# Kernel tuning notes

Measured on AMD Instinct MI355X. Metric: run time of the kernel, lower is better.

Reference implementation:

```python
import jax, jax.numpy as jnp
import numpy as np

B, T, IN_DIM, HID_DIM = 64, 1024, 256, 256


def setup_inputs() -> dict:
    key = jax.random.key(0)
    ks = jax.random.split(key, 5)
    glorot = np.sqrt(6.0 / (IN_DIM + HID_DIM * 2)).astype(np.float32)
    def W(k):
        return jax.random.uniform(k, (IN_DIM + HID_DIM, HID_DIM), jnp.float32, -glorot, glorot)
    return {
        "x": jax.random.normal(ks[0], (B, T, IN_DIM), jnp.float32),
        "W_i": W(ks[1]), "b_i": jnp.zeros((HID_DIM,), jnp.float32),
        "W_f": W(ks[2]), "b_f": jnp.zeros((HID_DIM,), jnp.float32),
        "W_o": W(ks[3]), "b_o": jnp.zeros((HID_DIM,), jnp.float32),
        "W_c": W(ks[4]), "b_c": jnp.zeros((HID_DIM,), jnp.float32),
    }


def reference(x, W_i, b_i, W_f, b_f, W_o, b_o, W_c, b_c):
    # x: [B, T, in_dim] -> time-major [T, B, in_dim]
    xt = jnp.transpose(x, (1, 0, 2))
    batch = x.shape[0]
    c0 = jnp.zeros((batch, HID_DIM), x.dtype)
    h0 = jnp.zeros((batch, HID_DIM), x.dtype)

    def step(carry, x_t):
        c, h = carry
        hx = jnp.concatenate([h, x_t], axis=1)  # [B, hid+in]
        i = jax.nn.sigmoid(hx @ W_i + b_i)
        f = jax.nn.sigmoid(hx @ W_f + b_f)
        o = jax.nn.sigmoid(hx @ W_o + b_o)
        c_new = f * c + i * jnp.tanh(hx @ W_c + b_c)
        h_new = o * jnp.tanh(c_new)
        return (c_new, h_new), h_new

    _, outputs = jax.lax.scan(step, (c0, h0), xt)
    return outputs  # [T, B, hid_dim]
```

## Files before the change

kernel.cpp:

```cpp
#include <hip/hip_runtime.h>
#include <hip/hip_fp16.h>
#include <cstdint>

typedef _Float16 f16x8 __attribute__((ext_vector_type(8)));
typedef _Float16 half2_t __attribute__((ext_vector_type(2)));
typedef float f32x4 __attribute__((ext_vector_type(4)));
typedef uint32_t u32x4 __attribute__((ext_vector_type(4)));


#define XG_OFF    0ULL
#define XG_BYTES  134217728ULL
#define AP_OFF    (XG_OFF + XG_BYTES)
#define AP_BYTES  33554432ULL
#define BP_OFF    (AP_OFF + AP_BYTES)
#define BP_BYTES  524288ULL
#define WHP_OFF   (BP_OFF + BP_BYTES)
#define WHP_BYTES 524288ULL
#define BIAS_OFF  (WHP_OFF + WHP_BYTES)

#define KRQ 28
#define KLB 113
#define KL  15

__device__ inline half2_t u2h2(uint32_t v) {
    union { uint32_t u; half2_t h; } c; c.u = v; return c.h;
}

#define QB(v, pat) __int_as_float(__builtin_amdgcn_ds_swizzle(__float_as_int(v), (pat)))

__global__ void pack_weights(const float* __restrict__ Wi, const float* __restrict__ Wf,
                             const float* __restrict__ Wo, const float* __restrict__ Wc,
                             const float* __restrict__ bi, const float* __restrict__ bf,
                             const float* __restrict__ bo, const float* __restrict__ bc,
                             uint32_t* __restrict__ Whp, __half* __restrict__ Bp,
                             float* __restrict__ bias_eff)
{
    int tidg = blockIdx.x * blockDim.x + threadIdx.x;
    if (tidg < 131072) {
        int c  = tidg & 1023;
        int kp = tidg >> 10;
        int u = c >> 2, g = c & 3;
        const float* W = (g == 0) ? Wi : (g == 1) ? Wf : (g == 2) ? Wo : Wc;
        union { uint32_t u32; __half h[2]; } pk;
        pk.h[0] = __float2half(W[(2 * kp) * 256 + u]);
        pk.h[1] = __float2half(W[(2 * kp + 1) * 256 + u]);
        Whp[tidg] = pk.u32;
    } else if (tidg < 131072 + 262144) {
        int beta = tidg - 131072;
        int i = beta & 7;
        int l = (beta >> 3) & 63;
        int kk = (beta >> 9) & 7;
        int n = beta >> 12;
        int c = n * 16 + (l & 15);
        int u = c >> 2, g = c & 3;
        int k = kk * 32 + (l >> 4) * 8 + i;
        const float* W = (g == 0) ? Wi : (g == 1) ? Wf : (g == 2) ? Wo : Wc;
        Bp[beta] = __float2half(W[(256 + k) * 256 + u]);
    } else if (tidg < 131072 + 262144 + 1024) {
        int c = tidg - (131072 + 262144);
        int g = c & 3;
        const float* bb = (g == 0) ? bi : (g == 1) ? bf : (g == 2) ? bo : bc;
        bias_eff[c] = bb[c >> 2];
    }
}

__global__ void pack_a(const float* __restrict__ x, __half* __restrict__ Ap)
{
    int t = blockIdx.x * blockDim.x + threadIdx.x;
    int l  = t & 63;
    int kk = (t >> 6) & 7;
    int m  = t >> 9;
    int row = m * 16 + (l & 15);
    int k0  = kk * 32 + (l >> 4) * 8;
    const float* src = x + (size_t)row * 256 + k0;
    f16x8 v;
#pragma unroll
    for (int i = 0; i < 8; ++i) v[i] = (_Float16)src[i];
    *reinterpret_cast<f16x8*>(Ap + (size_t)t * 8) = v;
}

__global__ __launch_bounds__(256) void gemm_xg(const __half* __restrict__ Ap,
                                               const __half* __restrict__ Bp,
                                               const float* __restrict__ bias_eff,
                                               __half* __restrict__ xg)
{
    int wave = threadIdx.x >> 6;
    int lane = threadIdx.x & 63;
    int mtile = blockIdx.x * 4 + wave;
    int ntbase = blockIdx.y * 16;

    f16x8 a[8];
#pragma unroll
    for (int kk = 0; kk < 8; ++kk)
        a[kk] = *reinterpret_cast<const f16x8*>(Ap + ((size_t)(mtile * 8 + kk) * 64 + lane) * 8);

    int col_lo = lane & 15;
    int rgrp = lane >> 4;
#pragma unroll 1
    for (int j = 0; j < 16; ++j) {
        int nt = ntbase + j;
        float bb = bias_eff[nt * 16 + col_lo];
        f32x4 acc = {bb, bb, bb, bb};
#pragma unroll
        for (int kk = 0; kk < 8; ++kk) {
            f16x8 bfr = *reinterpret_cast<const f16x8*>(Bp + ((size_t)(nt * 8 + kk) * 64 + lane) * 8);
            acc = __builtin_amdgcn_mfma_f32_16x16x32_f16(a[kk], bfr, acc, 0, 0, 0);
        }
#pragma unroll
        for (int r = 0; r < 4; ++r) {
            int row = mtile * 16 + rgrp * 4 + r;
            xg[(size_t)row * 1024 + nt * 16 + col_lo] = __float2half(acc[r]);
        }
    }
}

__global__ __launch_bounds__(512, 2) void lstm_rec(
    const __half* __restrict__ xg,
    const uint32_t* __restrict__ Whp,
    float* __restrict__ out)
{
    const int b = blockIdx.x;
    const int tid = threadIdx.x;
    const int g = tid & 3;
    const int ul = tid >> 2;

    __shared__ uint32_t Wl[KL][1024];
    __shared__ alignas(16) uint32_t h2[2][128];

    {
        const uint32_t* src = Whp + KLB * 1024;
        for (int i = tid; i < KL * 1024; i += 512) ((uint32_t*)Wl)[i] = src[i];
        if (tid < 128) { h2[0][tid] = 0u; h2[1][tid] = 0u; }
    }

    u32x4 w0[KRQ], w1[KRQ];
#pragma unroll
    for (int q = 0; q < KRQ; ++q) {
#pragma unroll
        for (int i = 0; i < 4; ++i) {
            w0[q][i] = Whp[(q * 4 + i) * 1024 + tid];
            w1[q][i] = Whp[(q * 4 + i) * 1024 + 512 + tid];
        }
    }
    uint32_t w0e = Whp[112 * 1024 + tid];
    uint32_t w1e = Whp[112 * 1024 + 512 + tid];
    __syncthreads();

    const float kAct = (g == 3) ? 2.88539008f : -1.44269504f;
    const float aAct = (g == 3) ? -2.0f : 1.0f;
    const float bAct = (g == 3) ? 1.0f : 0.0f;

    float c0s = 0.f, c1s = 0.f;
    const __half* xrow = xg + (size_t)b * 1024 * 1024;

    for (int t = 0; t < 1024; ++t) {
        const uint32_t* hr = h2[t & 1];
        float xv0 = (float)xrow[t * 1024 + tid];
        float xv1 = (float)xrow[t * 1024 + 512 + tid];

        float a00 = 0.f, a01 = 0.f, a10 = 0.f, a11 = 0.f;
#pragma unroll
        for (int q = 0; q < KRQ; ++q) {
            u32x4 hq = *reinterpret_cast<const u32x4*>(&hr[q * 4]);
            a00 = __builtin_amdgcn_fdot2(u2h2(w0[q][0]), u2h2(hq[0]), a00, false);
            a10 = __builtin_amdgcn_fdot2(u2h2(w1[q][0]), u2h2(hq[0]), a10, false);
            a01 = __builtin_amdgcn_fdot2(u2h2(w0[q][1]), u2h2(hq[1]), a01, false);
            a11 = __builtin_amdgcn_fdot2(u2h2(w1[q][1]), u2h2(hq[1]), a11, false);
            a00 = __builtin_amdgcn_fdot2(u2h2(w0[q][2]), u2h2(hq[2]), a00, false);
            a10 = __builtin_amdgcn_fdot2(u2h2(w1[q][2]), u2h2(hq[2]), a10, false);
            a01 = __builtin_amdgcn_fdot2(u2h2(w0[q][3]), u2h2(hq[3]), a01, false);
            a11 = __builtin_amdgcn_fdot2(u2h2(w1[q][3]), u2h2(hq[3]), a11, false);
        }
        {
            u32x4 hA = *reinterpret_cast<const u32x4*>(&hr[112]);
            u32x4 hB = *reinterpret_cast<const u32x4*>(&hr[116]);
            u32x4 hC = *reinterpret_cast<const u32x4*>(&hr[120]);
            u32x4 hD = *reinterpret_cast<const u32x4*>(&hr[124]);
            a00 = __builtin_amdgcn_fdot2(u2h2(w0e), u2h2(hA[0]), a00, false);
            a10 = __builtin_amdgcn_fdot2(u2h2(w1e), u2h2(hA[0]), a10, false);
#define LPART(J, HV) \
            a01 = __builtin_amdgcn_fdot2(u2h2(Wl[(J)][tid]), u2h2(HV), a01, false); \
            a11 = __builtin_amdgcn_fdot2(u2h2(Wl[(J)][512 + tid]), u2h2(HV), a11, false);
            LPART(0, hA[1]) LPART(1, hA[2]) LPART(2, hA[3])
            LPART(3, hB[0]) LPART(4, hB[1]) LPART(5, hB[2]) LPART(6, hB[3])
            LPART(7, hC[0]) LPART(8, hC[1]) LPART(9, hC[2]) LPART(10, hC[3])
            LPART(11, hD[0]) LPART(12, hD[1]) LPART(13, hD[2]) LPART(14, hD[3])
#undef LPART
        }

        float pre0 = (a00 + a01) + xv0;
        float pre1 = (a10 + a11) + xv1;

        float r0 = __builtin_amdgcn_rcpf(1.f + __builtin_amdgcn_exp2f(kAct * pre0));
        float r1 = __builtin_amdgcn_rcpf(1.f + __builtin_amdgcn_exp2f(kAct * pre1));
        float gv0 = fmaf(aAct, r0, bAct);
        float gv1 = fmaf(aAct, r1, bAct);

        float i0 = QB(gv0, 0x8000), f0 = QB(gv0, 0x8055), o0 = QB(gv0, 0x80AA), q0 = QB(gv0, 0x80FF);
        float i1 = QB(gv1, 0x8000), f1 = QB(gv1, 0x8055), o1 = QB(gv1, 0x80AA), q1 = QB(gv1, 0x80FF);

        c0s = fmaf(f0, c0s, i0 * q0);
        c1s = fmaf(f1, c1s, i1 * q1);
        float t0 = fmaf(-2.f, __builtin_amdgcn_rcpf(1.f + __builtin_amdgcn_exp2f(2.88539008f * c0s)), 1.f);
        float t1 = fmaf(-2.f, __builtin_amdgcn_rcpf(1.f + __builtin_amdgcn_exp2f(2.88539008f * c1s)), 1.f);
        float h0 = o0 * t0;
        float h1 = o1 * t1;

        __half* hw = reinterpret_cast<__half*>(h2[(t + 1) & 1]);
        if (g == 0) {
            hw[ul] = __float2half(h0);
            hw[128 + ul] = __float2half(h1);
        } else if (g == 1) {
            float* orow = out + ((size_t)t * 64 + b) * 256;
            orow[ul] = h0;
            orow[128 + ul] = h1;
        }
        __syncthreads();
    }
}

extern "C" void kernel_launch(void* const* d_in, const int* in_sizes, int n_in,
                              void* d_out, int out_size, void* d_ws, size_t ws_size,
                              hipStream_t stream)
{
    const float* x  = (const float*)d_in[0];
    const float* Wi = (const float*)d_in[1];
    const float* bi = (const float*)d_in[2];
    const float* Wf = (const float*)d_in[3];
    const float* bf = (const float*)d_in[4];
    const float* Wo = (const float*)d_in[5];
    const float* bo = (const float*)d_in[6];
    const float* Wc = (const float*)d_in[7];
    const float* bc = (const float*)d_in[8];

    char* ws = (char*)d_ws;
    __half*   xg       = (__half*)(ws + XG_OFF);
    __half*   Ap       = (__half*)(ws + AP_OFF);
    __half*   Bp       = (__half*)(ws + BP_OFF);
    uint32_t* Whp      = (uint32_t*)(ws + WHP_OFF);
    float*    bias_eff = (float*)(ws + BIAS_OFF);

    pack_weights<<<1540, 256, 0, stream>>>(Wi, Wf, Wo, Wc, bi, bf, bo, bc, Whp, Bp, bias_eff);
    pack_a<<<8192, 256, 0, stream>>>(x, Ap);
    gemm_xg<<<dim3(1024, 4), 256, 0, stream>>>(Ap, Bp, bias_eff, xg);
    lstm_rec<<<64, 512, 0, stream>>>(xg, Whp, (float*)d_out);
}
```

Before: 1.915 ms.

## Repartition recurrent weights between registers and LDS, interleave and prefetch gate inputs

```diff
diff --git a/kernel.cpp b/kernel.cpp
--- a/kernel.cpp
+++ b/kernel.cpp
@@ -6,6 +6,7 @@
 typedef _Float16 half2_t __attribute__((ext_vector_type(2)));
 typedef float f32x4 __attribute__((ext_vector_type(4)));
 typedef uint32_t u32x4 __attribute__((ext_vector_type(4)));
+typedef uint32_t u32x2 __attribute__((ext_vector_type(2)));
 
 
 #define XG_OFF    0ULL
@@ -14,37 +15,52 @@
 #define AP_BYTES  33554432ULL
 #define BP_OFF    (AP_OFF + AP_BYTES)
 #define BP_BYTES  524288ULL
-#define WHP_OFF   (BP_OFF + BP_BYTES)
-#define WHP_BYTES 524288ULL
-#define BIAS_OFF  (WHP_OFF + WHP_BYTES)
-
-#define KRQ 28
-#define KLB 113
-#define KL  15
+#define WHPQ_OFF  (BP_OFF + BP_BYTES)
+#define WHPQ_BYTES 425984ULL
+#define WLG_OFF   (WHPQ_OFF + WHPQ_BYTES)
+#define WLG_BYTES 98304ULL
+#define BIAS_OFF  (WLG_OFF + WLG_BYTES)
 
 __device__ inline half2_t u2h2(uint32_t v) {
     union { uint32_t u; half2_t h; } c; c.u = v; return c.h;
 }
-
+#define FD(W, H, A) __builtin_amdgcn_fdot2(u2h2(W), u2h2(H), (A), false)
 #define QB(v, pat) __int_as_float(__builtin_amdgcn_ds_swizzle(__float_as_int(v), (pat)))
+
+#define QLIST(F) F(0) F(1) F(2) F(3) F(4) F(5) F(6) F(7) F(8) F(9) F(10) F(11) F(12) \
+                 F(13) F(14) F(15) F(16) F(17) F(18) F(19) F(20) F(21) F(22) F(23) F(24) F(25)
 
 __global__ void pack_weights(const float* __restrict__ Wi, const float* __restrict__ Wf,
                              const float* __restrict__ Wo, const float* __restrict__ Wc,
                              const float* __restrict__ bi, const float* __restrict__ bf,
                              const float* __restrict__ bo, const float* __restrict__ bc,
-                             uint32_t* __restrict__ Whp, __half* __restrict__ Bp,
-                             float* __restrict__ bias_eff)
+                             uint32_t* __restrict__ WhpQ, uint32_t* __restrict__ WlG,
+                             __half* __restrict__ Bp, float* __restrict__ bias_eff)
 {
     int tidg = blockIdx.x * blockDim.x + threadIdx.x;
-    if (tidg < 131072) {
-        int c  = tidg & 1023;
-        int kp = tidg >> 10;
+    if (tidg < 106496) {
+        int i = tidg & 3;
+        int c = (tidg >> 2) & 1023;
+        int q = tidg >> 12;
+        int kp = q * 4 + i;
         int u = c >> 2, g = c & 3;
         const float* W = (g == 0) ? Wi : (g == 1) ? Wf : (g == 2) ? Wo : Wc;
         union { uint32_t u32; __half h[2]; } pk;
         pk.h[0] = __float2half(W[(2 * kp) * 256 + u]);
         pk.h[1] = __float2half(W[(2 * kp + 1) * 256 + u]);
-        Whp[tidg] = pk.u32;
+        WhpQ[tidg] = pk.u32;
+    } else if (tidg < 131072) {
+        int e = tidg - 106496;
+        int k = e & 1;
+        int c = (e >> 1) & 1023;
+        int jp = e >> 11;
+        int kp = 104 + 2 * jp + k;
+        int u = c >> 2, g = c & 3;
+        const float* W = (g == 0) ? Wi : (g == 1) ? Wf : (g == 2) ? Wo : Wc;
+        union { uint32_t u32; __half h[2]; } pk;
+        pk.h[0] = __float2half(W[(2 * kp) * 256 + u]);
+        pk.h[1] = __float2half(W[(2 * kp + 1) * 256 + u]);
+        WlG[e] = pk.u32;
     } else if (tidg < 131072 + 262144) {
         int beta = tidg - 131072;
         int i = beta & 7;
@@ -82,7 +98,7 @@
 __global__ __launch_bounds__(256) void gemm_xg(const __half* __restrict__ Ap,
                                                const __half* __restrict__ Bp,
                                                const float* __restrict__ bias_eff,
-                                               __half* __restrict__ xg)
+                                               __half* __restrict__ xgh)
 {
     int wave = threadIdx.x >> 6;
     int lane = threadIdx.x & 63;
@@ -99,24 +115,27 @@
 #pragma unroll 1
     for (int j = 0; j < 16; ++j) {
         int nt = ntbase + j;
-        float bb = bias_eff[nt * 16 + col_lo];
+        int c = nt * 16 + col_lo;
+        float bb = bias_eff[c];
         f32x4 acc = {bb, bb, bb, bb};
 #pragma unroll
         for (int kk = 0; kk < 8; ++kk) {
             f16x8 bfr = *reinterpret_cast<const f16x8*>(Bp + ((size_t)(nt * 8 + kk) * 64 + lane) * 8);
             acc = __builtin_amdgcn_mfma_f32_16x16x32_f16(a[kk], bfr, acc, 0, 0, 0);
         }
+        int hidx = ((c & 511) << 1) | (c >> 9);
 #pragma unroll
         for (int r = 0; r < 4; ++r) {
             int row = mtile * 16 + rgrp * 4 + r;
-            xg[(size_t)row * 1024 + nt * 16 + col_lo] = __float2half(acc[r]);
+            xgh[(size_t)row * 1024 + hidx] = __float2half(acc[r]);
         }
     }
 }
 
 __global__ __launch_bounds__(512, 2) void lstm_rec(
-    const __half* __restrict__ xg,
-    const uint32_t* __restrict__ Whp,
+    const uint32_t* __restrict__ xgp,
+    const uint32_t* __restrict__ WhpQ,
+    const uint32_t* __restrict__ WlG,
     float* __restrict__ out)
 {
     const int b = blockIdx.x;
@@ -124,26 +143,20 @@
     const int g = tid & 3;
     const int ul = tid >> 2;
 
-    __shared__ uint32_t Wl[KL][1024];
+    __shared__ uint32_t WlLDS[24576];
     __shared__ alignas(16) uint32_t h2[2][128];
 
-    {
-        const uint32_t* src = Whp + KLB * 1024;
-        for (int i = tid; i < KL * 1024; i += 512) ((uint32_t*)Wl)[i] = src[i];
-        if (tid < 128) { h2[0][tid] = 0u; h2[1][tid] = 0u; }
-    }
-
-    u32x4 w0[KRQ], w1[KRQ];
-#pragma unroll
-    for (int q = 0; q < KRQ; ++q) {
-#pragma unroll
-        for (int i = 0; i < 4; ++i) {
-            w0[q][i] = Whp[(q * 4 + i) * 1024 + tid];
-            w1[q][i] = Whp[(q * 4 + i) * 1024 + 512 + tid];
-        }
-    }
-    uint32_t w0e = Whp[112 * 1024 + tid];
-    uint32_t w1e = Whp[112 * 1024 + 512 + tid];
+    for (int i = tid; i < 24576; i += 512) WlLDS[i] = WlG[i];
+    if (tid < 128) { h2[0][tid] = 0u; h2[1][tid] = 0u; }
+
+#define DECLW(q) u32x4 w0_##q, w1_##q;
+    QLIST(DECLW)
+#undef DECLW
+#define LOADW(q) \
+    w0_##q = *reinterpret_cast<const u32x4*>(WhpQ + (((q) * 1024) + tid) * 4); \
+    w1_##q = *reinterpret_cast<const u32x4*>(WhpQ + (((q) * 1024) + 512 + tid) * 4);
+    QLIST(LOADW)
+#undef LOADW
     __syncthreads();
 
     const float kAct = (g == 3) ? 2.88539008f : -1.44269504f;
@@ -151,45 +164,48 @@
     const float bAct = (g == 3) ? 1.0f : 0.0f;
 
     float c0s = 0.f, c1s = 0.f;
-    const __half* xrow = xg + (size_t)b * 1024 * 1024;
+    const uint32_t* xrow = xgp + (size_t)b * 1024 * 512 + tid;
+    uint32_t xw = xrow[0];
 
     for (int t = 0; t < 1024; ++t) {
         const uint32_t* hr = h2[t & 1];
-        float xv0 = (float)xrow[t * 1024 + tid];
-        float xv1 = (float)xrow[t * 1024 + 512 + tid];
+        int tn = (t < 1023) ? (t + 1) : 1023;
+        uint32_t xw_next = xrow[(size_t)tn * 512];
 
         float a00 = 0.f, a01 = 0.f, a10 = 0.f, a11 = 0.f;
-#pragma unroll
-        for (int q = 0; q < KRQ; ++q) {
-            u32x4 hq = *reinterpret_cast<const u32x4*>(&hr[q * 4]);
-            a00 = __builtin_amdgcn_fdot2(u2h2(w0[q][0]), u2h2(hq[0]), a00, false);
-            a10 = __builtin_amdgcn_fdot2(u2h2(w1[q][0]), u2h2(hq[0]), a10, false);
-            a01 = __builtin_amdgcn_fdot2(u2h2(w0[q][1]), u2h2(hq[1]), a01, false);
-            a11 = __builtin_amdgcn_fdot2(u2h2(w1[q][1]), u2h2(hq[1]), a11, false);
-            a00 = __builtin_amdgcn_fdot2(u2h2(w0[q][2]), u2h2(hq[2]), a00, false);
-            a10 = __builtin_amdgcn_fdot2(u2h2(w1[q][2]), u2h2(hq[2]), a10, false);
-            a01 = __builtin_amdgcn_fdot2(u2h2(w0[q][3]), u2h2(hq[3]), a01, false);
-            a11 = __builtin_amdgcn_fdot2(u2h2(w1[q][3]), u2h2(hq[3]), a11, false);
-        }
+#define DOTQ(q) { \
+        u32x4 hq = *reinterpret_cast<const u32x4*>(hr + (q) * 4); \
+        a00 = FD(w0_##q[0], hq[0], a00); a10 = FD(w1_##q[0], hq[0], a10); \
+        a01 = FD(w0_##q[1], hq[1], a01); a11 = FD(w1_##q[1], hq[1], a11); \
+        a00 = FD(w0_##q[2], hq[2], a00); a10 = FD(w1_##q[2], hq[2], a10); \
+        a01 = FD(w0_##q[3], hq[3], a01); a11 = FD(w1_##q[3], hq[3], a11); }
+        QLIST(DOTQ)
+#undef DOTQ
+
         {
-            u32x4 hA = *reinterpret_cast<const u32x4*>(&hr[112]);
-            u32x4 hB = *reinterpret_cast<const u32x4*>(&hr[116]);
-            u32x4 hC = *reinterpret_cast<const u32x4*>(&hr[120]);
-            u32x4 hD = *reinterpret_cast<const u32x4*>(&hr[124]);
-            a00 = __builtin_amdgcn_fdot2(u2h2(w0e), u2h2(hA[0]), a00, false);
-            a10 = __builtin_amdgcn_fdot2(u2h2(w1e), u2h2(hA[0]), a10, false);
-#define LPART(J, HV) \
-            a01 = __builtin_amdgcn_fdot2(u2h2(Wl[(J)][tid]), u2h2(HV), a01, false); \
-            a11 = __builtin_amdgcn_fdot2(u2h2(Wl[(J)][512 + tid]), u2h2(HV), a11, false);
-            LPART(0, hA[1]) LPART(1, hA[2]) LPART(2, hA[3])
-            LPART(3, hB[0]) LPART(4, hB[1]) LPART(5, hB[2]) LPART(6, hB[3])
-            LPART(7, hC[0]) LPART(8, hC[1]) LPART(9, hC[2]) LPART(10, hC[3])
-            LPART(11, hD[0]) LPART(12, hD[1]) LPART(13, hD[2]) LPART(14, hD[3])
-#undef LPART
-        }
-
-        float pre0 = (a00 + a01) + xv0;
-        float pre1 = (a10 + a11) + xv1;
+            u32x4 hT0 = *reinterpret_cast<const u32x4*>(hr + 104);
+            u32x4 hT1 = *reinterpret_cast<const u32x4*>(hr + 108);
+            u32x4 hT2 = *reinterpret_cast<const u32x4*>(hr + 112);
+            u32x4 hT3 = *reinterpret_cast<const u32x4*>(hr + 116);
+            u32x4 hT4 = *reinterpret_cast<const u32x4*>(hr + 120);
+            u32x4 hT5 = *reinterpret_cast<const u32x4*>(hr + 124);
+#define TAILJP(jp, HA, HB) { \
+            u32x2 wl0 = *reinterpret_cast<const u32x2*>(&WlLDS[((jp) * 1024 + tid) * 2]); \
+            u32x2 wl1 = *reinterpret_cast<const u32x2*>(&WlLDS[((jp) * 1024 + 512 + tid) * 2]); \
+            a00 = FD(wl0[0], HA, a00); a01 = FD(wl0[1], HB, a01); \
+            a10 = FD(wl1[0], HA, a10); a11 = FD(wl1[1], HB, a11); }
+            TAILJP(0,  hT0[0], hT0[1])  TAILJP(1,  hT0[2], hT0[3])
+            TAILJP(2,  hT1[0], hT1[1])  TAILJP(3,  hT1[2], hT1[3])
+            TAILJP(4,  hT2[0], hT2[1])  TAILJP(5,  hT2[2], hT2[3])
+            TAILJP(6,  hT3[0], hT3[1])  TAILJP(7,  hT3[2], hT3[3])
+            TAILJP(8,  hT4[0], hT4[1])  TAILJP(9,  hT4[2], hT4[3])
+            TAILJP(10, hT5[0], hT5[1])  TAILJP(11, hT5[2], hT5[3])
+#undef TAILJP
+        }
+
+        union { uint32_t u; __half h[2]; } xc; xc.u = xw;
+        float pre0 = (a00 + a01) + __half2float(xc.h[0]);
+        float pre1 = (a10 + a11) + __half2float(xc.h[1]);
 
         float r0 = __builtin_amdgcn_rcpf(1.f + __builtin_amdgcn_exp2f(kAct * pre0));
         float r1 = __builtin_amdgcn_rcpf(1.f + __builtin_amdgcn_exp2f(kAct * pre1));
@@ -207,15 +223,15 @@
         float h1 = o1 * t1;
 
         __half* hw = reinterpret_cast<__half*>(h2[(t + 1) & 1]);
-        if (g == 0) {
-            hw[ul] = __float2half(h0);
-            hw[128 + ul] = __float2half(h1);
-        } else if (g == 1) {
+        if (g == 0)      hw[ul] = __float2half(h0);
+        else if (g == 2) hw[128 + ul] = __float2half(h1);
+        else if (g == 1) {
             float* orow = out + ((size_t)t * 64 + b) * 256;
             orow[ul] = h0;
             orow[128 + ul] = h1;
         }
         __syncthreads();
+        xw = xw_next;
     }
 }
 
@@ -234,14 +250,16 @@
     const float* bc = (const float*)d_in[8];
 
     char* ws = (char*)d_ws;
-    __half*   xg       = (__half*)(ws + XG_OFF);
+    __half*   xgh      = (__half*)(ws + XG_OFF);
+    uint32_t* xgp      = (uint32_t*)(ws + XG_OFF);
     __half*   Ap       = (__half*)(ws + AP_OFF);
     __half*   Bp       = (__half*)(ws + BP_OFF);
-    uint32_t* Whp      = (uint32_t*)(ws + WHP_OFF);
+    uint32_t* WhpQ     = (uint32_t*)(ws + WHPQ_OFF);
+    uint32_t* WlG      = (uint32_t*)(ws + WLG_OFF);
     float*    bias_eff = (float*)(ws + BIAS_OFF);
 
-    pack_weights<<<1540, 256, 0, stream>>>(Wi, Wf, Wo, Wc, bi, bf, bo, bc, Whp, Bp, bias_eff);
+    pack_weights<<<1540, 256, 0, stream>>>(Wi, Wf, Wo, Wc, bi, bf, bo, bc, WhpQ, WlG, Bp, bias_eff);
     pack_a<<<8192, 256, 0, stream>>>(x, Ap);
-    gemm_xg<<<dim3(1024, 4), 256, 0, stream>>>(Ap, Bp, bias_eff, xg);
-    lstm_rec<<<64, 512, 0, stream>>>(xg, Whp, (float*)d_out);
-}
+    gemm_xg<<<dim3(1024, 4), 256, 0, stream>>>(Ap, Bp, bias_eff, xgh);
+    lstm_rec<<<64, 512, 0, stream>>>(xgp, WhpQ, WlG, (float*)d_out);
+}
```

Measured after the change: 2.362 ms. 1.23x slower.
